# Kernel tuning notes

Hardware: AMD Instinct MI355X
Metric: run time of the kernel (lower is better)

Reference implementation:

```python
import jax, jax.numpy as jnp
import numpy as np

B, T, D = 64, 512, 1024

def setup_inputs() -> dict:
    key = jax.random.key(0)
    k1, k2, k3 = jax.random.split(key, 3)
    q1 = jax.random.normal(k1, (B, T, D), dtype=jnp.float32)
    q2 = jax.random.normal(k2, (B, T, D), dtype=jnp.float32)
    # original uses 'uniform' init; scale like a small uniform weight
    U = jax.random.uniform(k3, (D, D), dtype=jnp.float32, minval=-0.05, maxval=0.05)
    return {"q1": q1, "q2": q2, "U": U}

def reference(q1, q2, U):
    # bilinear scores: (q1 @ U) @ q2^T -> [B, T1, T2]
    att = jnp.einsum('btd,de,bse->bts', q1, U, q2)
    att = jax.nn.relu(att)
    w1_att = jax.nn.softmax(att, axis=1)  # softmax over q1 timesteps
    w2_att = jax.nn.softmax(att, axis=2)  # softmax over q2 timesteps
    # q1_align = w1_att^T @ q1 -> [B, T2, D]
    q1_align = jnp.einsum('bts,btd->bsd', w1_att, q1)
    # q2_align = w2_att @ q2 -> [B, T1, D]
    q2_align = jnp.einsum('bts,bsd->btd', w2_att, q2)
    return (q1_align, q2_align)
```

## Files before the change

kernel.cpp:

```cpp
#include <hip/hip_runtime.h>
#include <hip/hip_bf16.h>
#include <math.h>

#define B_DIM 64
#define T_DIM 512
#define D_DIM 1024
#define TT (T_DIM * T_DIM)
#define TD (T_DIM * D_DIM)

typedef _Float16 f16;
typedef f16 f16x4 __attribute__((ext_vector_type(4)));
typedef f16 f16x8 __attribute__((ext_vector_type(8)));
typedef float f32x4 __attribute__((ext_vector_type(4)));


__device__ __forceinline__ void gld_lds16(const void* g, void* l) {
    __builtin_amdgcn_global_load_lds(
        (const __attribute__((address_space(1))) void*)g,
        (__attribute__((address_space(3))) void*)l, 16, 0, 0);
}

template <int EPI>
__global__ __launch_bounds__(512, 2) void k_mfma2(
        const f16* __restrict__ A, int lda,
        const f16* __restrict__ Bt, int ldb, int K,
        void* __restrict__ Cout, int ldc,
        const float* __restrict__ scale,
        long batchA, long batchB, long batchC, long batchS) {
    __shared__ f16 LA[2][8192];
    __shared__ f16 LB[2][8192];

    const int tid = threadIdx.x;
    const int lane = tid & 63, w = tid >> 6;

    const int gX = gridDim.x, gY = gridDim.y;
    int nwg = gX * gY * gridDim.z;
    int o = blockIdx.x + gX * (blockIdx.y + gY * blockIdx.z);
    int q8 = nwg >> 3, r8 = nwg & 7, xcd = o & 7, idx = o >> 3;
    int fl = (xcd < r8 ? xcd * (q8 + 1) : r8 * (q8 + 1) + (xcd - r8) * q8) + idx;
    const int bx = fl % gX;
    int tmp = fl / gX;
    const int by = tmp % gY;
    const int bz = tmp / gY;

    const f16* Ab = A + (long)bz * batchA + (long)(by * 256) * lda;
    const f16* Bb = Bt + (long)bz * batchB + (long)(bx * 256) * ldb;

    const int r0 = tid >> 2, s0 = (tid & 3) ^ (r0 & 3);
    const int r1 = (512 + tid) >> 2, s1 = ((512 + tid) & 3) ^ (r1 & 3);
    const long offA0 = (long)r0 * lda + s0 * 8;
    const long offA1 = (long)r1 * lda + s1 * 8;
    const long offB0 = (long)r0 * ldb + s0 * 8;
    const long offB1 = (long)r1 * ldb + s1 * 8;
    const int ldsOff0 = w * 512;
    const int ldsOff1 = 4096 + w * 512;

    const int g = lane >> 4;
    const int rA0 = (w & 1) * 128 + (lane & 15);
    const int rB0 = (w >> 1) * 64 + (lane & 15);

    f32x4 acc[8][4] = {};

    gld_lds16(Ab + offA0, &LA[0][ldsOff0]);
    gld_lds16(Ab + offA1, &LA[0][ldsOff1]);
    gld_lds16(Bb + offB0, &LB[0][ldsOff0]);
    gld_lds16(Bb + offB1, &LB[0][ldsOff1]);
    __syncthreads();

    const int NT = K >> 5;
    for (int t = 0; t < NT; ++t) {
        const int cur = t & 1;
        if (t + 1 < NT) {
            const long kt = (long)(t + 1) << 5;
            gld_lds16(Ab + offA0 + kt, &LA[cur ^ 1][ldsOff0]);
            gld_lds16(Ab + offA1 + kt, &LA[cur ^ 1][ldsOff1]);
            gld_lds16(Bb + offB0 + kt, &LB[cur ^ 1][ldsOff0]);
            gld_lds16(Bb + offB1 + kt, &LB[cur ^ 1][ldsOff1]);
        }
        f16x8 a[8], b[4];
#pragma unroll
        for (int m = 0; m < 8; ++m) {
            int r = rA0 + m * 16;
            a[m] = *(const f16x8*)(&LA[cur][r * 32 + ((g ^ (r & 3)) << 3)]);
        }
#pragma unroll
        for (int n = 0; n < 4; ++n) {
            int r = rB0 + n * 16;
            b[n] = *(const f16x8*)(&LB[cur][r * 32 + ((g ^ (r & 3)) << 3)]);
        }
#pragma unroll
        for (int m = 0; m < 8; ++m)
#pragma unroll
            for (int n = 0; n < 4; ++n)
                acc[m][n] = __builtin_amdgcn_mfma_f32_16x16x32_f16(a[m], b[n], acc[m][n], 0, 0, 0);
        __syncthreads();
    }

    const int row0 = by * 256 + (w & 1) * 128 + (lane >> 4) * 4;
    const int col0 = bx * 256 + (w >> 1) * 64 + (lane & 15);
    if constexpr (EPI == 0) {
        f16* C = (f16*)Cout;
#pragma unroll
        for (int m = 0; m < 8; ++m)
#pragma unroll
            for (int r = 0; r < 4; ++r) {
                long row = row0 + m * 16 + r;
#pragma unroll
                for (int n = 0; n < 4; ++n)
                    C[row * ldc + col0 + n * 16] = (f16)acc[m][n][r];
            }
    } else if constexpr (EPI == 1) {
        float* C = (float*)Cout + (long)bz * batchC;
#pragma unroll
        for (int m = 0; m < 8; ++m)
#pragma unroll
            for (int r = 0; r < 4; ++r) {
                long row = row0 + m * 16 + r;
#pragma unroll
                for (int n = 0; n < 4; ++n)
                    C[row * ldc + col0 + n * 16] = fmaxf(acc[m][n][r], 0.0f);
            }
    } else {
        float* C = (float*)Cout + (long)bz * batchC;
        const float* sz = scale + (long)bz * batchS;
#pragma unroll
        for (int m = 0; m < 8; ++m)
#pragma unroll
            for (int r = 0; r < 4; ++r) {
                long row = row0 + m * 16 + r;
                float inv = 1.0f / sz[row];
#pragma unroll
                for (int n = 0; n < 4; ++n)
                    C[row * ldc + col0 + n * 16] = acc[m][n][r] * inv;
            }
    }
}

__global__ __launch_bounds__(256) void k_cast_both(const float* __restrict__ src,
                                                   f16* __restrict__ dst,
                                                   f16* __restrict__ dstT) {
    __shared__ f16 tr[64][72];
    int b = blockIdx.z;
    int d0 = blockIdx.x * 64, t0 = blockIdx.y * 64;
    const float* S = src + ((size_t)b * T_DIM + t0) * D_DIM + d0;
    f16* Dr = dst + ((size_t)b * T_DIM + t0) * D_DIM + d0;
    int tid = threadIdx.x;
    int rr = tid >> 4, cc = (tid & 15) * 4;
#pragma unroll
    for (int i = 0; i < 4; ++i) {
        int r = rr + i * 16;
        float4 v = *(const float4*)(S + (size_t)r * D_DIM + cc);
        f16x4 h = {(f16)v.x, (f16)v.y, (f16)v.z, (f16)v.w};
        *(f16x4*)(Dr + (size_t)r * D_DIM + cc) = h;
        tr[cc + 0][r] = h[0];
        tr[cc + 1][r] = h[1];
        tr[cc + 2][r] = h[2];
        tr[cc + 3][r] = h[3];
    }
    __syncthreads();
    f16* Dt = dstT + ((size_t)b * D_DIM + d0) * T_DIM + t0;
    int r2 = tid >> 3, c8 = (tid & 7) * 8;
#pragma unroll
    for (int i = 0; i < 2; ++i) {
        int d = r2 + i * 32;
        f16x8 vv = *(const f16x8*)(&tr[d][c8]);
        *(f16x8*)(Dt + (size_t)d * T_DIM + c8) = vv;
    }
}

__global__ __launch_bounds__(256) void k_castU(const float* __restrict__ U,
                                               f16* __restrict__ Uht) {
    __shared__ f16 tr[64][72];
    int n0 = blockIdx.x * 64, k0 = blockIdx.y * 64;
    int tid = threadIdx.x;
    int rr = tid >> 4, cc = (tid & 15) * 4;
#pragma unroll
    for (int i = 0; i < 4; ++i) {
        int r = rr + i * 16;
        float4 v = *(const float4*)(U + (size_t)(k0 + r) * D_DIM + n0 + cc);
        tr[cc + 0][r] = (f16)v.x;
        tr[cc + 1][r] = (f16)v.y;
        tr[cc + 2][r] = (f16)v.z;
        tr[cc + 3][r] = (f16)v.w;
    }
    __syncthreads();
    int r2 = tid >> 3, c8 = (tid & 7) * 8;
#pragma unroll
    for (int i = 0; i < 2; ++i) {
        int n = r2 + i * 32;
        f16x8 vv = *(const f16x8*)(&tr[n][c8]);
        *(f16x8*)(Uht + (size_t)(n0 + n) * D_DIM + k0 + c8) = vv;
    }
}

__global__ __launch_bounds__(256) void k_pconv(const float* __restrict__ att,
                                               const float* __restrict__ rmax,
                                               const float* __restrict__ cmax,
                                               f16* __restrict__ P2, f16* __restrict__ P1,
                                               int b0) {
    __shared__ f16 tr[64][72];
    int z = blockIdx.z;
    int t0 = blockIdx.y * 64, s0 = blockIdx.x * 64;
    const float* S = att + (size_t)z * TT + (size_t)t0 * T_DIM + s0;
    const float* rm = rmax + (size_t)(b0 + z) * T_DIM + t0;
    const float* cm = cmax + (size_t)(b0 + z) * T_DIM + s0;
    int tid = threadIdx.x;
    int rr = tid >> 4, cc = (tid & 15) * 4;
#pragma unroll
    for (int i = 0; i < 4; ++i) {
        int r = rr + i * 16;
        float4 v = *(const float4*)(S + (size_t)r * T_DIM + cc);
        float m = rm[r];
        f16x4 p2 = {(f16)__expf(v.x - m), (f16)__expf(v.y - m),
                    (f16)__expf(v.z - m), (f16)__expf(v.w - m)};
        *(f16x4*)(P2 + (size_t)z * TT + (size_t)(t0 + r) * T_DIM + s0 + cc) = p2;
        float4 c4 = *(const float4*)(cm + cc);
        tr[cc + 0][r] = (f16)__expf(v.x - c4.x);
        tr[cc + 1][r] = (f16)__expf(v.y - c4.y);
        tr[cc + 2][r] = (f16)__expf(v.z - c4.z);
        tr[cc + 3][r] = (f16)__expf(v.w - c4.w);
    }
    __syncthreads();
    int r2 = tid >> 3, c8 = (tid & 7) * 8;
#pragma unroll
    for (int i = 0; i < 2; ++i) {
        int s = r2 + i * 32;
        f16x8 vv = *(const f16x8*)(&tr[s][c8]);
        *(f16x8*)(P1 + (size_t)z * TT + (size_t)(s0 + s) * T_DIM + t0 + c8) = vv;
    }
}

__global__ __launch_bounds__(256) void k_rowstats(const float* __restrict__ att,
                                                  float* __restrict__ rmax,
                                                  float* __restrict__ rsum, int b0) {
    int wave = threadIdx.x >> 6, lane = threadIdx.x & 63;
    int lr = blockIdx.x * 4 + wave;
    const float4* row = reinterpret_cast<const float4*>(att + (size_t)lr * T_DIM);
    float4 v0 = row[lane];
    float4 v1 = row[lane + 64];
    float m = fmaxf(fmaxf(fmaxf(v0.x, v0.y), fmaxf(v0.z, v0.w)),
                    fmaxf(fmaxf(v1.x, v1.y), fmaxf(v1.z, v1.w)));
#pragma unroll
    for (int off = 32; off >= 1; off >>= 1) m = fmaxf(m, __shfl_xor(m, off));
    float s = __expf(v0.x - m) + __expf(v0.y - m) + __expf(v0.z - m) + __expf(v0.w - m)
            + __expf(v1.x - m) + __expf(v1.y - m) + __expf(v1.z - m) + __expf(v1.w - m);
#pragma unroll
    for (int off = 32; off >= 1; off >>= 1) s += __shfl_xor(s, off);
    if (lane == 0) {
        size_t gr = (size_t)b0 * T_DIM + lr;
        rmax[gr] = m;
        rsum[gr] = s;
    }
}

__global__ __launch_bounds__(256) void k_colstats(const float* __restrict__ att,
                                                  float* __restrict__ cmax,
                                                  float* __restrict__ csum, int b0) {
    int lb = blockIdx.y;
    int s = blockIdx.x * 256 + threadIdx.x;
    const float* base = att + (size_t)lb * TT + s;
    float m = -INFINITY, sum = 0.f;
    for (int t = 0; t < T_DIM; ++t) {
        float x = base[(size_t)t * T_DIM];
        float nm = fmaxf(m, x);
        sum = sum * __expf(m - nm) + __expf(x - nm);
        m = nm;
    }
    size_t g = (size_t)(b0 + lb) * T_DIM + s;
    cmax[g] = m;
    csum[g] = sum;
}

#define BM 128
#define BN 128
#define BKK 16
#define APITCH 132

__device__ __forceinline__ void stage_a_rowmajor(float* As, const float* __restrict__ A,
                                                 int lda, int tid) {
#pragma unroll
    for (int i = 0; i < 2; ++i) {
        int idx = tid + i * 256;
        int r = idx >> 2;
        int k4 = (idx & 3) << 2;
        float4 v = *reinterpret_cast<const float4*>(&A[(size_t)r * lda + k4]);
        As[(k4 + 0) * APITCH + r] = v.x;
        As[(k4 + 1) * APITCH + r] = v.y;
        As[(k4 + 2) * APITCH + r] = v.z;
        As[(k4 + 3) * APITCH + r] = v.w;
    }
}
__device__ __forceinline__ void stage_a_rowmajor_exp(float* As, const float* __restrict__ A,
                                                     int lda, const float* __restrict__ rowmax,
                                                     int tid) {
#pragma unroll
    for (int i = 0; i < 2; ++i) {
        int idx = tid + i * 256;
        int r = idx >> 2;
        int k4 = (idx & 3) << 2;
        float4 v = *reinterpret_cast<const float4*>(&A[(size_t)r * lda + k4]);
        float m = rowmax[r];
        As[(k4 + 0) * APITCH + r] = __expf(v.x - m);
        As[(k4 + 1) * APITCH + r] = __expf(v.y - m);
        As[(k4 + 2) * APITCH + r] = __expf(v.z - m);
        As[(k4 + 3) * APITCH + r] = __expf(v.w - m);
    }
}
__device__ __forceinline__ void stage_a_colmajor_exp(float* As, const float* __restrict__ S,
                                                     int lds, const float* __restrict__ colmax,
                                                     int tid) {
#pragma unroll
    for (int i = 0; i < 2; ++i) {
        int idx = tid + i * 256;
        int k = idx >> 5;
        int m4 = (idx & 31) << 2;
        float4 v = *reinterpret_cast<const float4*>(&S[(size_t)k * lds + m4]);
        float4 c = *reinterpret_cast<const float4*>(&colmax[m4]);
        float4 o;
        o.x = __expf(v.x - c.x); o.y = __expf(v.y - c.y);
        o.z = __expf(v.z - c.z); o.w = __expf(v.w - c.w);
        *reinterpret_cast<float4*>(&As[k * APITCH + m4]) = o;
    }
}
__device__ __forceinline__ void stage_b_rowmajor(float* Bs, const float* __restrict__ Bp,
                                                 int ldb, int tid) {
#pragma unroll
    for (int i = 0; i < 2; ++i) {
        int idx = tid + i * 256;
        int k = idx >> 5;
        int c4 = idx & 31;
        float4 v = *reinterpret_cast<const float4*>(&Bp[(size_t)k * ldb + (c4 << 2)]);
        *reinterpret_cast<float4*>(&Bs[k * BN + ((c4 & 1) << 6) + ((c4 >> 1) << 2)]) = v;
    }
}
__device__ __forceinline__ void stage_b_transpose(float* Bs, const float* __restrict__ Q,
                                                  int ldq, int tid) {
#pragma unroll
    for (int i = 0; i < 2; ++i) {
        int idx = tid + i * 256;
        int s = idx >> 2;
        int e4 = (idx & 3) << 2;
        float4 v = *reinterpret_cast<const float4*>(&Q[(size_t)s * ldq + e4]);
        int sw = ((s & 4) << 4) + ((s >> 3) << 2) + (s & 3);
        Bs[(e4 + 0) * BN + sw] = v.x;
        Bs[(e4 + 1) * BN + sw] = v.y;
        Bs[(e4 + 2) * BN + sw] = v.z;
        Bs[(e4 + 3) * BN + sw] = v.w;
    }
}
__device__ __forceinline__ void gemm_inner(const float* As, const float* Bs,
                                           float acc[8][8], int tx, int ty) {
#pragma unroll
    for (int k = 0; k < BKK; ++k) {
        float4 a0 = *reinterpret_cast<const float4*>(&As[k * APITCH + ty * 8]);
        float4 a1 = *reinterpret_cast<const float4*>(&As[k * APITCH + ty * 8 + 4]);
        float4 b0 = *reinterpret_cast<const float4*>(&Bs[k * BN + tx * 4]);
        float4 b1 = *reinterpret_cast<const float4*>(&Bs[k * BN + 64 + tx * 4]);
        float a[8] = {a0.x, a0.y, a0.z, a0.w, a1.x, a1.y, a1.z, a1.w};
        float b[8] = {b0.x, b0.y, b0.z, b0.w, b1.x, b1.y, b1.z, b1.w};
#pragma unroll
        for (int i = 0; i < 8; ++i)
#pragma unroll
            for (int j = 0; j < 8; ++j)
                acc[i][j] = fmaf(a[i], b[j], acc[i][j]);
    }
}
__global__ __launch_bounds__(256) void k_gemm_qU(const float* __restrict__ q1,
                                                 const float* __restrict__ U,
                                                 float* __restrict__ qU, int b0) {
    __shared__ float As[BKK * APITCH];
    __shared__ float Bs[BKK * BN];
    int tid = threadIdx.x, tx = tid & 15, ty = tid >> 4;
    int m0 = blockIdx.y * BM;
    int n0 = blockIdx.x * BN;
    const float* Abase = q1 + (size_t)b0 * TD + (size_t)m0 * D_DIM;
    const float* Bbase = U + n0;
    float acc[8][8] = {};
    for (int kt = 0; kt < D_DIM; kt += BKK) {
        stage_a_rowmajor(As, Abase + kt, D_DIM, tid);
        stage_b_rowmajor(Bs, Bbase + (size_t)kt * D_DIM, D_DIM, tid);
        __syncthreads();
        gemm_inner(As, Bs, acc, tx, ty);
        __syncthreads();
    }
    float* Cp = qU + (size_t)m0 * D_DIM + n0;
#pragma unroll
    for (int i = 0; i < 8; ++i) {
        int r = ty * 8 + i;
        float4 o0 = {acc[i][0], acc[i][1], acc[i][2], acc[i][3]};
        float4 o1 = {acc[i][4], acc[i][5], acc[i][6], acc[i][7]};
        *reinterpret_cast<float4*>(&Cp[(size_t)r * D_DIM + tx * 8]) = o0;
        *reinterpret_cast<float4*>(&Cp[(size_t)r * D_DIM + tx * 8 + 4]) = o1;
    }
}
__global__ __launch_bounds__(256) void k_att(const float* __restrict__ qU,
                                             const float* __restrict__ q2,
                                             float* __restrict__ att, int b0) {
    __shared__ float As[BKK * APITCH];
    __shared__ float Bs[BKK * BN];
    int tid = threadIdx.x, tx = tid & 15, ty = tid >> 4;
    int lb = blockIdx.z;
    int m0 = blockIdx.y * BM;
    int n0 = blockIdx.x * BN;
    const float* Abase = qU + (size_t)lb * TD + (size_t)m0 * D_DIM;
    const float* Qbase = q2 + (size_t)(b0 + lb) * TD + (size_t)n0 * D_DIM;
    float acc[8][8] = {};
    for (int kt = 0; kt < D_DIM; kt += BKK) {
        stage_a_rowmajor(As, Abase + kt, D_DIM, tid);
        stage_b_transpose(Bs, Qbase + kt, D_DIM, tid);
        __syncthreads();
        gemm_inner(As, Bs, acc, tx, ty);
        __syncthreads();
    }
    float* Cp = att + (size_t)lb * TT + (size_t)m0 * T_DIM + n0;
#pragma unroll
    for (int i = 0; i < 8; ++i) {
        int r = ty * 8 + i;
        float4 o0 = {fmaxf(acc[i][0], 0.f), fmaxf(acc[i][1], 0.f), fmaxf(acc[i][2], 0.f), fmaxf(acc[i][3], 0.f)};
        float4 o1 = {fmaxf(acc[i][4], 0.f), fmaxf(acc[i][5], 0.f), fmaxf(acc[i][6], 0.f), fmaxf(acc[i][7], 0.f)};
        *reinterpret_cast<float4*>(&Cp[(size_t)r * T_DIM + tx * 8]) = o0;
        *reinterpret_cast<float4*>(&Cp[(size_t)r * T_DIM + tx * 8 + 4]) = o1;
    }
}
__global__ __launch_bounds__(256) void k_q2align(const float* __restrict__ att,
                                                 const float* __restrict__ q2,
                                                 const float* __restrict__ rmax,
                                                 const float* __restrict__ rsum,
                                                 float* __restrict__ out, int b0) {
    __shared__ float As[BKK * APITCH];
    __shared__ float Bs[BKK * BN];
    int tid = threadIdx.x, tx = tid & 15, ty = tid >> 4;
    int lb = blockIdx.z;
    int m0 = blockIdx.y * BM;
    int n0 = blockIdx.x * BN;
    const float* Abase = att + (size_t)lb * TT + (size_t)m0 * T_DIM;
    const float* rmaxp = rmax + (size_t)(b0 + lb) * T_DIM + m0;
    const float* rsump = rsum + (size_t)(b0 + lb) * T_DIM + m0;
    const float* Bbase = q2 + (size_t)(b0 + lb) * TD + n0;
    float acc[8][8] = {};
    for (int kt = 0; kt < T_DIM; kt += BKK) {
        stage_a_rowmajor_exp(As, Abase + kt, T_DIM, rmaxp, tid);
        stage_b_rowmajor(Bs, Bbase + (size_t)kt * D_DIM, D_DIM, tid);
        __syncthreads();
        gemm_inner(As, Bs, acc, tx, ty);
        __syncthreads();
    }
    float* Cp = out + (size_t)B_DIM * TD + (size_t)(b0 + lb) * TD + (size_t)m0 * D_DIM + n0;
#pragma unroll
    for (int i = 0; i < 8; ++i) {
        int r = ty * 8 + i;
        float inv = 1.0f / rsump[r];
        float4 o0 = {acc[i][0] * inv, acc[i][1] * inv, acc[i][2] * inv, acc[i][3] * inv};
        float4 o1 = {acc[i][4] * inv, acc[i][5] * inv, acc[i][6] * inv, acc[i][7] * inv};
        *reinterpret_cast<float4*>(&Cp[(size_t)r * D_DIM + tx * 8]) = o0;
        *reinterpret_cast<float4*>(&Cp[(size_t)r * D_DIM + tx * 8 + 4]) = o1;
    }
}
__global__ __launch_bounds__(256) void k_q1align(const float* __restrict__ att,
                                                 const float* __restrict__ q1,
                                                 const float* __restrict__ cmax,
                                                 const float* __restrict__ csum,
                                                 float* __restrict__ out, int b0) {
    __shared__ float As[BKK * APITCH];
    __shared__ float Bs[BKK * BN];
    int tid = threadIdx.x, tx = tid & 15, ty = tid >> 4;
    int lb = blockIdx.z;
    int m0 = blockIdx.y * BM;
    int n0 = blockIdx.x * BN;
    const float* Sbase = att + (size_t)lb * TT + m0;
    const float* cmaxp = cmax + (size_t)(b0 + lb) * T_DIM + m0;
    const float* csump = csum + (size_t)(b0 + lb) * T_DIM + m0;
    const float* Bbase = q1 + (size_t)(b0 + lb) * TD + n0;
    float acc[8][8] = {};
    for (int kt = 0; kt < T_DIM; kt += BKK) {
        stage_a_colmajor_exp(As, Sbase + (size_t)kt * T_DIM, T_DIM, cmaxp, tid);
        stage_b_rowmajor(Bs, Bbase + (size_t)kt * D_DIM, D_DIM, tid);
        __syncthreads();
        gemm_inner(As, Bs, acc, tx, ty);
        __syncthreads();
    }
    float* Cp = out + (size_t)(b0 + lb) * TD + (size_t)m0 * D_DIM + n0;
#pragma unroll
    for (int i = 0; i < 8; ++i) {
        int r = ty * 8 + i;
        float inv = 1.0f / csump[r];
        float4 o0 = {acc[i][0] * inv, acc[i][1] * inv, acc[i][2] * inv, acc[i][3] * inv};
        float4 o1 = {acc[i][4] * inv, acc[i][5] * inv, acc[i][6] * inv, acc[i][7] * inv};
        *reinterpret_cast<float4*>(&Cp[(size_t)r * D_DIM + tx * 8]) = o0;
        *reinterpret_cast<float4*>(&Cp[(size_t)r * D_DIM + tx * 8 + 4]) = o1;
    }
}

extern "C" void kernel_launch(void* const* d_in, const int* in_sizes, int n_in,
                              void* d_out, int out_size, void* d_ws, size_t ws_size,
                              hipStream_t stream) {
    const float* q1 = (const float*)d_in[0];
    const float* q2 = (const float*)d_in[1];
    const float* U  = (const float*)d_in[2];
    float* out = (float*)d_out;

    const size_t BT  = (size_t)B_DIM * T_DIM;
    const size_t BTD = (size_t)B_DIM * TD;
    const size_t DD  = (size_t)D_DIM * D_DIM;

    const size_t fixedB = BT * 4 * 4
                        + (4 * BTD + DD) * 2;
    const size_t perbB  = (size_t)TD * 2 + (size_t)TT * 4 + (size_t)TT * 4;
    int C = 64;
    while (C > 1 && fixedB + (size_t)C * perbB > ws_size) C >>= 1;

    if (fixedB + perbB <= ws_size) {
        float* rmax = (float*)d_ws;
        float* rsum = rmax + BT;
        float* cmax = rsum + BT;
        float* csum = cmax + BT;
        f16* q1h  = (f16*)(csum + BT);
        f16* q1ht = q1h  + BTD;
        f16* q2h  = q1ht + BTD;
        f16* q2ht = q2h  + BTD;
        f16* Uht  = q2ht + BTD;
        f16* qUh  = Uht  + DD;
        float* att = (float*)(qUh + (size_t)C * TD);
        f16* P2h  = (f16*)(att + (size_t)C * TT);
        f16* P1h  = P2h + (size_t)C * TT;

        k_cast_both<<<dim3(16, 8, 64), 256, 0, stream>>>(q1, q1h, q1ht);
        k_cast_both<<<dim3(16, 8, 64), 256, 0, stream>>>(q2, q2h, q2ht);
        k_castU<<<dim3(16, 16), 256, 0, stream>>>(U, Uht);

        for (int b0 = 0; b0 < B_DIM; b0 += C) {
            k_mfma2<0><<<dim3(4, C * 2, 1), 512, 0, stream>>>(
                q1h + (size_t)b0 * TD, D_DIM, Uht, D_DIM, D_DIM,
                qUh, D_DIM, nullptr, 0, 0, 0, 0);
            k_mfma2<1><<<dim3(2, 2, C), 512, 0, stream>>>(
                qUh, D_DIM, q2h + (size_t)b0 * TD, D_DIM, D_DIM,
                att, T_DIM, nullptr, (long)TD, (long)TD, (long)TT, 0);
            k_rowstats<<<dim3(C * T_DIM / 4), 256, 0, stream>>>(att, rmax, rsum, b0);
            k_colstats<<<dim3(T_DIM / 256, C), 256, 0, stream>>>(att, cmax, csum, b0);
            k_pconv<<<dim3(8, 8, C), 256, 0, stream>>>(att, rmax, cmax, P2h, P1h, b0);
            k_mfma2<2><<<dim3(4, 2, C), 512, 0, stream>>>(
                P2h, T_DIM, q2ht + (size_t)b0 * TD, T_DIM, T_DIM,
                out + BTD + (size_t)b0 * TD, D_DIM, rsum + (size_t)b0 * T_DIM,
                (long)TT, (long)TD, (long)TD, T_DIM);
            k_mfma2<3><<<dim3(4, 2, C), 512, 0, stream>>>(
                P1h, T_DIM, q1ht + (size_t)b0 * TD, T_DIM, T_DIM,
                out + (size_t)b0 * TD, D_DIM, csum + (size_t)b0 * T_DIM,
                (long)TT, (long)TD, (long)TD, T_DIM);
        }
        return;
    }

    const size_t statsElems = 4ull * B_DIM * T_DIM;
    float* rmax = (float*)d_ws;
    float* rsum = rmax + BT;
    float* cmax = rsum + BT;
    float* csum = cmax + BT;
    float* scratch = csum + BT;
    size_t availFloats = (ws_size > statsElems * 4) ? (ws_size - statsElems * 4) / 4 : 0;
    int C2 = 64;
    while (C2 > 1 && (size_t)C2 * (TD + TT) > availFloats) C2 >>= 1;
    if ((size_t)C2 * (TD + TT) > availFloats) return;
    float* qU  = scratch;
    float* att = qU + (size_t)C2 * TD;
    for (int b0 = 0; b0 < B_DIM; b0 += C2) {
        k_gemm_qU<<<dim3(D_DIM / BN, C2 * (T_DIM / BM)), 256, 0, stream>>>(q1, U, qU, b0);
        k_att<<<dim3(T_DIM / BN, T_DIM / BM, C2), 256, 0, stream>>>(qU, q2, att, b0);
        k_rowstats<<<dim3(C2 * T_DIM / 4), 256, 0, stream>>>(att, rmax, rsum, b0);
        k_colstats<<<dim3(T_DIM / 256, C2), 256, 0, stream>>>(att, cmax, csum, b0);
        k_q2align<<<dim3(D_DIM / BN, T_DIM / BM, C2), 256, 0, stream>>>(att, q2, rmax, rsum, out, b0);
        k_q1align<<<dim3(D_DIM / BN, T_DIM / BM, C2), 256, 0, stream>>>(att, q1, cmax, csum, out, b0);
    }
}
```

Before: 483.7 us.

## Fuse softmax row/col stats into score GEMM epilogue and merge alignment GEMMs

The relu score GEMM epilogue now computes per-tile row and column max/sum-exp partials through warp shuffles and an LDS reduction, and writes them to small partial buffers. A tiny combine kernel merges the two partials per row and column, which replaces the separate rowstats and colstats passes that re-read the full attention matrix. The two final alignment GEMMs are launched as one grid with a doubled z dimension, selecting operands by z index, to improve occupancy and remove one launch. This adds epilogue work and LDS traffic to the score GEMM.

```diff
diff --git a/kernel.cpp b/kernel.cpp
--- a/kernel.cpp
+++ b/kernel.cpp
@@ -26,7 +26,10 @@
         const f16* __restrict__ Bt, int ldb, int K,
         void* __restrict__ Cout, int ldc,
         const float* __restrict__ scale,
-        long batchA, long batchB, long batchC, long batchS) {
+        long batchA, long batchB, long batchC, long batchS,
+        float2* __restrict__ rowP, float2* __restrict__ colP, long pstr,
+        const f16* __restrict__ A2, const f16* __restrict__ Bt2,
+        void* __restrict__ Cout2, const float* __restrict__ scale2, int zsplit) {
     __shared__ f16 LA[2][8192];
     __shared__ f16 LB[2][8192];
 
@@ -43,8 +46,18 @@
     const int by = tmp % gY;
     const int bz = tmp / gY;
 
-    const f16* Ab = A + (long)bz * batchA + (long)(by * 256) * lda;
-    const f16* Bb = Bt + (long)bz * batchB + (long)(bx * 256) * ldb;
+    const f16* Au = A; const f16* Bu = Bt;
+    void* Cu = Cout; const float* su = scale;
+    int zb = bz;
+    if constexpr (EPI == 2) {
+        if (bz >= zsplit) {
+            zb = bz - zsplit;
+            Au = A2; Bu = Bt2; Cu = Cout2; su = scale2;
+        }
+    }
+
+    const f16* Ab = Au + (long)zb * batchA + (long)(by * 256) * lda;
+    const f16* Bb = Bu + (long)zb * batchB + (long)(bx * 256) * ldb;
 
     const int r0 = tid >> 2, s0 = (tid & 3) ^ (r0 & 3);
     const int r1 = (512 + tid) >> 2, s1 = ((512 + tid) & 3) ^ (r1 & 3);
@@ -98,8 +111,9 @@
 
     const int row0 = by * 256 + (w & 1) * 128 + (lane >> 4) * 4;
     const int col0 = bx * 256 + (w >> 1) * 64 + (lane & 15);
+
     if constexpr (EPI == 0) {
-        f16* C = (f16*)Cout;
+        f16* C = (f16*)Cu;
 #pragma unroll
         for (int m = 0; m < 8; ++m)
 #pragma unroll
@@ -110,7 +124,14 @@
                     C[row * ldc + col0 + n * 16] = (f16)acc[m][n][r];
             }
     } else if constexpr (EPI == 1) {
-        float* C = (float*)Cout + (long)bz * batchC;
+#pragma unroll
+        for (int m = 0; m < 8; ++m)
+#pragma unroll
+            for (int n = 0; n < 4; ++n)
+#pragma unroll
+                for (int r = 0; r < 4; ++r)
+                    acc[m][n][r] = fmaxf(acc[m][n][r], 0.0f);
+        float* C = (float*)Cu + (long)zb * batchC;
 #pragma unroll
         for (int m = 0; m < 8; ++m)
 #pragma unroll
@@ -118,11 +139,78 @@
                 long row = row0 + m * 16 + r;
 #pragma unroll
                 for (int n = 0; n < 4; ++n)
-                    C[row * ldc + col0 + n * 16] = fmaxf(acc[m][n][r], 0.0f);
+                    C[row * ldc + col0 + n * 16] = acc[m][n][r];
             }
+        float* redR = (float*)(&LA[0][0]);
+        float* redC = redR + 2048;
+        const int h = w & 1, cw = w >> 1;
+#pragma unroll
+        for (int m = 0; m < 8; ++m)
+#pragma unroll
+            for (int r = 0; r < 4; ++r) {
+                float mx = fmaxf(fmaxf(acc[m][0][r], acc[m][1][r]),
+                                 fmaxf(acc[m][2][r], acc[m][3][r]));
+                mx = fmaxf(mx, __shfl_xor(mx, 1));
+                mx = fmaxf(mx, __shfl_xor(mx, 2));
+                mx = fmaxf(mx, __shfl_xor(mx, 4));
+                mx = fmaxf(mx, __shfl_xor(mx, 8));
+                float sm = __expf(acc[m][0][r] - mx) + __expf(acc[m][1][r] - mx)
+                         + __expf(acc[m][2][r] - mx) + __expf(acc[m][3][r] - mx);
+                sm += __shfl_xor(sm, 1);
+                sm += __shfl_xor(sm, 2);
+                sm += __shfl_xor(sm, 4);
+                sm += __shfl_xor(sm, 8);
+                if ((lane & 15) == 0) {
+                    int lr = m * 16 + (lane >> 4) * 4 + r;
+                    redR[((h * 128 + lr) * 4 + cw) * 2 + 0] = mx;
+                    redR[((h * 128 + lr) * 4 + cw) * 2 + 1] = sm;
+                }
+            }
+#pragma unroll
+        for (int n = 0; n < 4; ++n) {
+            float mx = acc[0][n][0];
+#pragma unroll
+            for (int m = 0; m < 8; ++m)
+#pragma unroll
+                for (int r = 0; r < 4; ++r) mx = fmaxf(mx, acc[m][n][r]);
+            mx = fmaxf(mx, __shfl_xor(mx, 16));
+            mx = fmaxf(mx, __shfl_xor(mx, 32));
+            float sm = 0.f;
+#pragma unroll
+            for (int m = 0; m < 8; ++m)
+#pragma unroll
+                for (int r = 0; r < 4; ++r) sm += __expf(acc[m][n][r] - mx);
+            sm += __shfl_xor(sm, 16);
+            sm += __shfl_xor(sm, 32);
+            if (lane < 16) {
+                int c = cw * 64 + n * 16 + lane;
+                redC[(h * 256 + c) * 2 + 0] = mx;
+                redC[(h * 256 + c) * 2 + 1] = sm;
+            }
+        }
+        __syncthreads();
+        if (tid < 256) {
+            float M = -1e30f, S = 0.f;
+#pragma unroll
+            for (int i = 0; i < 4; ++i) {
+                float m_ = redR[(tid * 4 + i) * 2 + 0];
+                float s_ = redR[(tid * 4 + i) * 2 + 1];
+                float nm = fmaxf(M, m_);
+                S = S * __expf(M - nm) + s_ * __expf(m_ - nm);
+                M = nm;
+            }
+            rowP[(long)bx * pstr + (long)bz * 512 + by * 256 + tid] = make_float2(M, S);
+        } else {
+            int c = tid - 256;
+            float m0_ = redC[c * 2 + 0], s0_ = redC[c * 2 + 1];
+            float m1_ = redC[(256 + c) * 2 + 0], s1_ = redC[(256 + c) * 2 + 1];
+            float M = fmaxf(m0_, m1_);
+            float S = s0_ * __expf(m0_ - M) + s1_ * __expf(m1_ - M);
+            colP[(long)by * pstr + (long)bz * 512 + bx * 256 + c] = make_float2(M, S);
+        }
     } else {
-        float* C = (float*)Cout + (long)bz * batchC;
-        const float* sz = scale + (long)bz * batchS;
+        float* C = (float*)Cu + (long)zb * batchC;
+        const float* sz = su + (long)zb * batchS;
 #pragma unroll
         for (int m = 0; m < 8; ++m)
 #pragma unroll
@@ -134,6 +222,25 @@
                     C[row * ldc + col0 + n * 16] = acc[m][n][r] * inv;
             }
     }
+}
+
+__global__ __launch_bounds__(256) void k_comb(const float2* __restrict__ rowP,
+                                              const float2* __restrict__ colP, long pstr,
+                                              float* __restrict__ rmax, float* __restrict__ rsum,
+                                              float* __restrict__ cmax, float* __restrict__ csum,
+                                              int b0, int n) {
+    int i = blockIdx.x * 256 + threadIdx.x;
+    if (i >= n) return;
+    float2 a = rowP[i], b = rowP[pstr + i];
+    float M = fmaxf(a.x, b.x);
+    float S = a.y * __expf(a.x - M) + b.y * __expf(b.x - M);
+    rmax[(size_t)b0 * T_DIM + i] = M;
+    rsum[(size_t)b0 * T_DIM + i] = S;
+    a = colP[i]; b = colP[pstr + i];
+    M = fmaxf(a.x, b.x);
+    S = a.y * __expf(a.x - M) + b.y * __expf(b.x - M);
+    cmax[(size_t)b0 * T_DIM + i] = M;
+    csum[(size_t)b0 * T_DIM + i] = S;
 }
 
 __global__ __launch_bounds__(256) void k_cast_both(const float* __restrict__ src,
@@ -505,7 +612,8 @@
 
     const size_t fixedB = BT * 4 * 4
                         + (4 * BTD + DD) * 2;
-    const size_t perbB  = (size_t)TD * 2 + (size_t)TT * 4 + (size_t)TT * 4;
+    const size_t perbB  = (size_t)TD * 2 + (size_t)TT * 4 + (size_t)TT * 4
+                        + 4ull * T_DIM * sizeof(float2);
     int C = 64;
     while (C > 1 && fixedB + (size_t)C * perbB > ws_size) C >>= 1;
 
@@ -523,6 +631,9 @@
         float* att = (float*)(qUh + (size_t)C * TD);
         f16* P2h  = (f16*)(att + (size_t)C * TT);
         f16* P1h  = P2h + (size_t)C * TT;
+        float2* rowP = (float2*)(P1h + (size_t)C * TT);
+        float2* colP = rowP + 2ull * C * T_DIM;
+        const long pstr = (long)C * T_DIM;
 
         k_cast_both<<<dim3(16, 8, 64), 256, 0, stream>>>(q1, q1h, q1ht);
         k_cast_both<<<dim3(16, 8, 64), 256, 0, stream>>>(q2, q2h, q2ht);
@@ -531,21 +642,22 @@
         for (int b0 = 0; b0 < B_DIM; b0 += C) {
             k_mfma2<0><<<dim3(4, C * 2, 1), 512, 0, stream>>>(
                 q1h + (size_t)b0 * TD, D_DIM, Uht, D_DIM, D_DIM,
-                qUh, D_DIM, nullptr, 0, 0, 0, 0);
+                qUh, D_DIM, nullptr, 0, 0, 0, 0,
+                nullptr, nullptr, 0, nullptr, nullptr, nullptr, nullptr, 0);
             k_mfma2<1><<<dim3(2, 2, C), 512, 0, stream>>>(
                 qUh, D_DIM, q2h + (size_t)b0 * TD, D_DIM, D_DIM,
-                att, T_DIM, nullptr, (long)TD, (long)TD, (long)TT, 0);
-            k_rowstats<<<dim3(C * T_DIM / 4), 256, 0, stream>>>(att, rmax, rsum, b0);
-            k_colstats<<<dim3(T_DIM / 256, C), 256, 0, stream>>>(att, cmax, csum, b0);
+                att, T_DIM, nullptr, (long)TD, (long)TD, (long)TT, 0,
+                rowP, colP, pstr, nullptr, nullptr, nullptr, nullptr, 0);
+            k_comb<<<dim3((C * T_DIM + 255) / 256), 256, 0, stream>>>(
+                rowP, colP, pstr, rmax, rsum, cmax, csum, b0, C * T_DIM);
             k_pconv<<<dim3(8, 8, C), 256, 0, stream>>>(att, rmax, cmax, P2h, P1h, b0);
-            k_mfma2<2><<<dim3(4, 2, C), 512, 0, stream>>>(
+            k_mfma2<2><<<dim3(4, 2, 2 * C), 512, 0, stream>>>(
                 P2h, T_DIM, q2ht + (size_t)b0 * TD, T_DIM, T_DIM,
                 out + BTD + (size_t)b0 * TD, D_DIM, rsum + (size_t)b0 * T_DIM,
-                (long)TT, (long)TD, (long)TD, T_DIM);
-            k_mfma2<3><<<dim3(4, 2, C), 512, 0, stream>>>(
-                P1h, T_DIM, q1ht + (size_t)b0 * TD, T_DIM, T_DIM,
-                out + (size_t)b0 * TD, D_DIM, csum + (size_t)b0 * T_DIM,
-                (long)TT, (long)TD, (long)TD, T_DIM);
+                (long)TT, (long)TD, (long)TD, T_DIM,
+                nullptr, nullptr, 0,
+                P1h, q1ht + (size_t)b0 * TD,
+                out + (size_t)b0 * TD, csum + (size_t)b0 * T_DIM, C);
         }
         return;
     }
```

Result: faster. 451.8 us (-6.6%).
